# Performance work log

Hardware: AMD Instinct MI355X
Metric: run time of the kernel (lower is better)

The kernel has to match this reference:

```python
import jax, jax.numpy as jnp
import numpy as np

B = 64
SIZES = [5023, 1256, 314, 79, 20]
NV = [s + 1 for s in SIZES]          # vertex counts incl. padding vertex
K = 12                               # spiral length (all levels)
LAT = 128
ENC_F = [3, 16, 32, 64, 128]
DEC_IN = [128, 64, 32, 32, 16]
DEC_OUT = [64, 32, 32, 16, 3]


def setup_inputs() -> dict:
    keys = iter(jax.random.split(jax.random.key(0), 80))

    def nrm(shape, scale=1.0):
        return jax.random.normal(next(keys), shape, jnp.float32) * scale

    inp = {}
    inp['x_talking'] = nrm((B, NV[0], 3))
    inp['template'] = nrm((B, NV[0], 3))
    for i in range(4):
        inp['D%d' % i] = nrm((NV[i + 1], NV[i]), 1.0 / np.sqrt(NV[i]))
        inp['U%d' % i] = nrm((NV[i], NV[i + 1]), 1.0 / np.sqrt(NV[i + 1]))
    for i in range(4):
        fan = ENC_F[i] * K
        inp['enc_w%d' % i] = nrm((ENC_F[i + 1], fan), 1.0 / np.sqrt(fan))
        inp['enc_b%d' % i] = jnp.zeros((ENC_F[i + 1],), jnp.float32)
    inp['fc_enc_w'] = nrm((LAT, NV[4] * DEC_IN[0]), 1.0 / np.sqrt(NV[4] * DEC_IN[0]))
    inp['fc_enc_b'] = jnp.zeros((LAT,), jnp.float32)
    inp['fc_dec_w'] = nrm((NV[4] * DEC_IN[0], 2 * LAT), 1.0 / np.sqrt(2 * LAT))
    inp['fc_dec_b'] = jnp.zeros((NV[4] * DEC_IN[0],), jnp.float32)
    for i in range(5):
        fan = DEC_IN[i] * K
        inp['dec_w%d' % i] = nrm((DEC_OUT[i], fan), 1.0 / np.sqrt(fan))
        inp['dec_b%d' % i] = jnp.zeros((DEC_OUT[i],), jnp.float32)
    for i in range(4):
        inp['S%d' % i] = jax.random.randint(next(keys), (NV[i], K), 0, NV[i], jnp.int32)
    return inp


def _spiral_conv(x, S, W, b, act):
    # x: [B, N, F]; S: [N, K] spiral neighbor indices; W: [out, K*F] (torch Linear layout)
    Bv, Nv, F = x.shape
    g = x[:, S, :].reshape(Bv, Nv, K * F)            # spiral neighbor gather
    y = act(jnp.einsum('bnf,of->bno', g, W) + b)     # gather-GEMM + activation
    mask = jnp.ones((1, Nv, 1), y.dtype).at[0, -1, 0].set(0.0)  # zero out padding vertex
    return y * mask


def _forward(x_talking, template, D, U, enc, fc_enc_w, fc_enc_b, fc_dec_w, fc_dec_b, dec, S):
    elu = jax.nn.elu
    # encode_talking
    x = x_talking
    for i in range(4):
        x = _spiral_conv(x, S[i], enc[i][0], enc[i][1], elu)
        x = jnp.einsum('mn,bnf->bmf', D[i], x)       # downsample
    z = x.reshape(B, -1) @ fc_enc_w.T + fc_enc_b     # [B, latent]
    # decode(z, z)
    h = jnp.concatenate([z, z], axis=1) @ fc_dec_w.T + fc_dec_b
    x = h.reshape(B, NV[4], DEC_IN[0])
    for i in range(3):
        x = jnp.einsum('mn,bnf->bmf', U[3 - i], x)   # upsample
        x = _spiral_conv(x, S[3 - i], dec[i][0], dec[i][1], elu)
    x = jnp.einsum('mn,bnf->bmf', U[0], x)
    x = _spiral_conv(x, S[0], dec[3][0], dec[3][1], elu)
    x = _spiral_conv(x, S[0], dec[4][0], dec[4][1], lambda v: v)  # identity activation
    return x, x + template


def reference(x_talking, template, D0, D1, D2, D3, U0, U1, U2, U3,
              enc_w0, enc_b0, enc_w1, enc_b1, enc_w2, enc_b2, enc_w3, enc_b3,
              fc_enc_w, fc_enc_b, fc_dec_w, fc_dec_b,
              dec_w0, dec_b0, dec_w1, dec_b1, dec_w2, dec_b2, dec_w3, dec_b3, dec_w4, dec_b4,
              S0, S1, S2, S3):
    return _forward(
        x_talking, template,
        [D0, D1, D2, D3], [U0, U1, U2, U3],
        [(enc_w0, enc_b0), (enc_w1, enc_b1), (enc_w2, enc_b2), (enc_w3, enc_b3)],
        fc_enc_w, fc_enc_b, fc_dec_w, fc_dec_b,
        [(dec_w0, dec_b0), (dec_w1, dec_b1), (dec_w2, dec_b2), (dec_w3, dec_b3), (dec_w4, dec_b4)],
        [S0, S1, S2, S3])
```

## Files before the change

### kernel.cpp

```cpp
#include <hip/hip_runtime.h>
#include <cstddef>


#define BATCH 64
#define SPK 12

typedef __attribute__((ext_vector_type(8))) short bf16x8;
typedef __attribute__((ext_vector_type(4))) short bf16x4;
typedef __attribute__((ext_vector_type(4))) float f32x4;

__device__ __forceinline__ unsigned short f2bf(float x) {
    union { float f; unsigned int u; } v; v.f = x;
    unsigned int r = v.u + 0x7FFF + ((v.u >> 16) & 1);
    return (unsigned short)(r >> 16);
}

__global__ __launch_bounds__(256) void f32_to_bf16_kernel(
    const float* __restrict__ in, unsigned short* __restrict__ out, int n8)
{
    int i = blockIdx.x * 256 + threadIdx.x;
    if (i < n8) {
        const float* p = in + (size_t)i * 8;
        bf16x8 r;
#pragma unroll
        for (int j = 0; j < 8; ++j) r[j] = (short)f2bf(p[j]);
        *(bf16x8*)(out + (size_t)i * 8) = r;
    }
}

__global__ __launch_bounds__(256) void a_bf16_pad_kernel(
    const float* __restrict__ A, unsigned short* __restrict__ Ap,
    int M, int K, int Kp, int total)
{
    int i = blockIdx.x * 256 + threadIdx.x;
    if (i >= total) return;
    int kp8 = Kp >> 3;
    int m = i / kp8;
    int k0 = (i - m * kp8) * 8;
    bf16x8 r;
    if (m < M) {
        const float* src = A + (size_t)m * K + k0;
#pragma unroll
        for (int j = 0; j < 8; ++j) {
            float v = (k0 + j < K) ? src[j] : 0.f;
            r[j] = (short)f2bf(v);
        }
    } else {
#pragma unroll
        for (int j = 0; j < 8; ++j) r[j] = 0;
    }
    *(bf16x8*)(Ap + (size_t)m * Kp + k0) = r;
}

template<int LOGF, int OBF16>
__global__ __launch_bounds__(64) void conv_wmfma_kernel(
    const unsigned short* __restrict__ x, const int* __restrict__ S,
    const unsigned short* __restrict__ Wb, const float* __restrict__ bias,
    void* __restrict__ yv, int Nv, int O, int elu_flag, int swz)
{
    constexpr int F  = 1 << LOGF;
    constexpr int KF = SPK * F;
    constexpr int NS = KF / 32;
    const int lane = threadIdx.x;
    const int l15  = lane & 15;
    const int quad = lane >> 4;

    int bx = blockIdx.x, by = blockIdx.y, bz = blockIdx.z;
    if (swz) {
        const int gx = gridDim.x, gy = gridDim.y;
        const int total = gx * gy * gridDim.z;
        int bid = bx + gx * (by + gy * bz);
        const int chunk = total >> 3;
        int sid = (bid & 7) * chunk + (bid >> 3);
        bx = sid % gx; sid /= gx;
        by = sid % gy;
        bz = sid / gy;
    }

    const int n0   = bx * 16;
    const int o    = by * 16 + l15;
    const int b    = bz;
    const size_t xb = (size_t)b * Nv;

    const int n  = n0 + l15;
    const int ng = (n < Nv) ? n : 0;
    const unsigned short* wrow = Wb + (size_t)o * KF;

    f32x4 acc0 = (f32x4){0.f, 0.f, 0.f, 0.f};
    f32x4 acc1 = (f32x4){0.f, 0.f, 0.f, 0.f};
#pragma unroll
    for (int s = 0; s < NS; ++s) {
        int kf  = s * 32 + quad * 8;
        int k   = kf >> LOGF;
        int f   = kf & (F - 1);
        int src = S[ng * SPK + k];
        bf16x8 a = *(const bf16x8*)(x + ((xb + src) << LOGF) + f);
        bf16x8 w = *(const bf16x8*)(wrow + kf);
        if (s & 1) acc1 = __builtin_amdgcn_mfma_f32_16x16x32_bf16(a, w, acc1, 0, 0, 0);
        else       acc0 = __builtin_amdgcn_mfma_f32_16x16x32_bf16(a, w, acc0, 0, 0, 0);
    }
    float bv = bias[o];
#pragma unroll
    for (int reg = 0; reg < 4; ++reg) {
        int nn = n0 + quad * 4 + reg;
        if (nn >= Nv) continue;
        float v = acc0[reg] + acc1[reg] + bv;
        if (elu_flag && v <= 0.f) v = expm1f(v);
        if (nn == Nv - 1) v = 0.f;
        size_t off = ((size_t)b * Nv + nn) * O + o;
        if (OBF16) ((unsigned short*)yv)[off] = f2bf(v);
        else       ((float*)yv)[off] = v;
    }
}

template<int LOGF>
__global__ __launch_bounds__(256) void conv_mfma32_kernel(
    const unsigned short* __restrict__ x, const int* __restrict__ S,
    const unsigned short* __restrict__ Wb, const float* __restrict__ bias,
    float* __restrict__ y, int Nv, int KF, int elu_flag)
{
    constexpr int PAD = 40;
    __shared__ unsigned short Gs[2][256 * PAD];

    const int b    = blockIdx.x;
    const int n0   = blockIdx.y * 256;
    const int tid  = threadIdx.x;
    const int lane = tid & 63;
    const int wave = tid >> 6;
    const int wm   = wave * 64;
    const int l15  = lane & 15;
    const int quad = lane >> 4;
    const size_t xb = (size_t)b * Nv;
    const int nslab = KF >> 5;

    f32x4 acc[4][2];
#pragma unroll
    for (int t = 0; t < 4; ++t)
#pragma unroll
        for (int o = 0; o < 2; ++o) acc[t][o] = (f32x4){0.f, 0.f, 0.f, 0.f};

    auto gath = [&](int k0, bf16x8* g) {
        int n = n0 + tid;
        if (n < Nv) {
#pragma unroll
            for (int j = 0; j < 4; ++j) {
                int kf  = k0 + j * 8;
                int k   = kf >> LOGF;
                int f   = kf & ((1 << LOGF) - 1);
                int src = S[n * SPK + k];
                g[j] = *(const bf16x8*)(x + ((xb + src) << LOGF) + f);
            }
        } else {
#pragma unroll
            for (int j = 0; j < 4; ++j)
#pragma unroll
                for (int e = 0; e < 8; ++e) g[j][e] = 0;
        }
    };
    auto put = [&](int buf, const bf16x8* g) {
#pragma unroll
        for (int j = 0; j < 4; ++j)
            *(bf16x8*)&Gs[buf][tid * PAD + j * 8] = g[j];
    };
    auto wfrag = [&](int k0, int o16) {
        return *(const bf16x8*)(Wb + (size_t)(o16 * 16 + l15) * KF + k0 + quad * 8);
    };

    bf16x8 gcur[4], gnext[4];
    gath(0, gcur);
    put(0, gcur);
    __syncthreads();

    for (int s = 0; s < nslab; ++s) {
        const int cur = s & 1;
        const bool more = (s + 1) < nslab;
        if (more) gath((s + 1) * 32, gnext);
        bf16x8 wf0 = wfrag(s * 32, 0);
        bf16x8 wf1 = wfrag(s * 32, 1);
#pragma unroll
        for (int t = 0; t < 4; ++t) {
            bf16x8 a = *(const bf16x8*)&Gs[cur][(wm + t * 16 + l15) * PAD + quad * 8];
            acc[t][0] = __builtin_amdgcn_mfma_f32_16x16x32_bf16(a, wf0, acc[t][0], 0, 0, 0);
            acc[t][1] = __builtin_amdgcn_mfma_f32_16x16x32_bf16(a, wf1, acc[t][1], 0, 0, 0);
        }
        if (more) {
            put(cur ^ 1, gnext);
            __syncthreads();
        }
    }

    float bv0 = bias[l15];
    float bv1 = bias[16 + l15];
#pragma unroll
    for (int t = 0; t < 4; ++t)
#pragma unroll
        for (int reg = 0; reg < 4; ++reg) {
            int n = n0 + wm + t * 16 + quad * 4 + reg;
            if (n >= Nv) continue;
            float v0 = acc[t][0][reg] + bv0;
            float v1 = acc[t][1][reg] + bv1;
            if (elu_flag) {
                if (v0 <= 0.f) v0 = expm1f(v0);
                if (v1 <= 0.f) v1 = expm1f(v1);
            }
            if (n == Nv - 1) { v0 = 0.f; v1 = 0.f; }
            size_t off = ((size_t)b * Nv + n) * 32 + l15;
            y[off]      = v0;
            y[off + 16] = v1;
        }
}

__global__ __launch_bounds__(256) void dsamp_mfma3_kernel(
    const unsigned short* __restrict__ Ab, const unsigned short* __restrict__ Xt,
    float* __restrict__ Y, int M, int Kp, int logF, int kchunk,
    int atomic_flag, int swz)
{
    constexpr int PAD = 40;
    __shared__ unsigned short As[2][128 * PAD];
    __shared__ unsigned short Bs[2][128 * PAD];

    int bx = blockIdx.x, by = blockIdx.y, bz = blockIdx.z;
    if (swz) {
        const int gx = gridDim.x, gy = gridDim.y;
        const int total = gx * gy * gridDim.z;
        int bid = bx + gx * (by + gy * bz);
        const int chunk = total >> 3;
        int sid = (bid & 7) * chunk + (bid >> 3);
        bx = sid % gx; sid /= gx;
        by = sid % gy;
        bz = sid / gy;
    }

    const int fmask = (1 << logF) - 1;
    const int m0   = bx * 128;
    const int c0   = by * 128;
    const int kbeg = bz * kchunk;
    int kend = kbeg + kchunk; if (kend > Kp) kend = Kp;
    const int nslab = (kend - kbeg + 31) >> 5;

    const int tid  = threadIdx.x;
    const int lane = tid & 63;
    const int wave = tid >> 6;
    const int wm   = (wave >> 1) * 64;
    const int wn   = (wave & 1) * 64;
    const int l15  = lane & 15;
    const int quad = lane >> 4;

    const int s_row = tid >> 2;
    const int s_k8  = (tid & 3) * 8;

    f32x4 acc[4][4];
#pragma unroll
    for (int i = 0; i < 4; ++i)
#pragma unroll
        for (int j = 0; j < 4; ++j) acc[i][j] = (f32x4){0.f, 0.f, 0.f, 0.f};

    bf16x8 apre[2], bpre[2];

    auto loadAB = [&](int ko) {
        apre[0] = *(const bf16x8*)(Ab + (size_t)(m0 + s_row)      * Kp + ko + s_k8);
        apre[1] = *(const bf16x8*)(Ab + (size_t)(m0 + s_row + 64) * Kp + ko + s_k8);
        bpre[0] = *(const bf16x8*)(Xt + (size_t)(c0 + s_row)      * Kp + ko + s_k8);
        bpre[1] = *(const bf16x8*)(Xt + (size_t)(c0 + s_row + 64) * Kp + ko + s_k8);
    };
    auto stage = [&](int buf) {
        *(bf16x8*)&As[buf][s_row * PAD + s_k8]        = apre[0];
        *(bf16x8*)&As[buf][(s_row + 64) * PAD + s_k8] = apre[1];
        *(bf16x8*)&Bs[buf][s_row * PAD + s_k8]        = bpre[0];
        *(bf16x8*)&Bs[buf][(s_row + 64) * PAD + s_k8] = bpre[1];
    };

    loadAB(kbeg);
    stage(0);
    __syncthreads();

    for (int s = 0; s < nslab; ++s) {
        const int cur = s & 1;
        const bool more = (s + 1) < nslab;
        if (more) loadAB(kbeg + (s + 1) * 32);

        bf16x8 af[4], bfr[4];
#pragma unroll
        for (int t = 0; t < 4; ++t) {
            af[t]  = *(const bf16x8*)&As[cur][(wm + t * 16 + l15) * PAD + quad * 8];
            bfr[t] = *(const bf16x8*)&Bs[cur][(wn + t * 16 + l15) * PAD + quad * 8];
        }
#pragma unroll
        for (int tm = 0; tm < 4; ++tm)
#pragma unroll
            for (int tn = 0; tn < 4; ++tn)
                acc[tm][tn] = __builtin_amdgcn_mfma_f32_16x16x32_bf16(af[tm], bfr[tn], acc[tm][tn], 0, 0, 0);

        if (more) { stage(cur ^ 1); __syncthreads(); }
    }

#pragma unroll
    for (int tm = 0; tm < 4; ++tm)
#pragma unroll
        for (int tn = 0; tn < 4; ++tn)
#pragma unroll
            for (int reg = 0; reg < 4; ++reg) {
                int m  = m0 + wm + tm * 16 + quad * 4 + reg;
                int cc = c0 + wn + tn * 16 + l15;
                if (m < M) {
                    int bb = cc >> logF, f = cc & fmask;
                    float* dst = Y + (((size_t)bb * M + m) << logF) + f;
                    if (atomic_flag) atomicAdd(dst, acc[tm][tn][reg]);
                    else *dst = acc[tm][tn][reg];
                }
            }
}

__global__ __launch_bounds__(256) void dsamp_mfma2_kernel(
    const unsigned short* __restrict__ Ap, const float* __restrict__ X,
    float* __restrict__ Y, int M, int K, int Kp, int logF, int kchunk,
    int atomic_flag)
{
    constexpr int PAD = 40;
    __shared__ unsigned short Xs[2][64 * PAD];

    const int fmask = (1 << logF) - 1;
    const int m0   = blockIdx.x * 64;
    const int c0   = blockIdx.y * 64;
    const int kbeg = blockIdx.z * kchunk;
    int kend = kbeg + kchunk; if (kend > K) kend = K;
    const int nslab = (kend - kbeg + 31) >> 5;

    const int tid  = threadIdx.x;
    const int lane = tid & 63;
    const int wave = tid >> 6;
    const int wm   = (wave >> 1) * 32;
    const int wn   = (wave & 1) * 32;
    const int l15  = lane & 15;
    const int quad = lane >> 4;

    const int skk  = tid >> 4;
    const int scg  = (tid & 15) * 4;
    const int cB   = c0 + scg;
    const int xbb  = cB >> logF;
    const int xf   = cB & fmask;
    const size_t xrowbase = (((size_t)xbb * K) << logF) + xf;

    const int mA0 = m0 + wm + l15;
    const int mA1 = mA0 + 16;
    const int kaoff = quad * 8;

    f32x4 acc[2][2];
    acc[0][0] = acc[0][1] = acc[1][0] = acc[1][1] = (f32x4){0.f, 0.f, 0.f, 0.f};

    float4 xn0, xn1;
    bf16x8 ac0, ac1, an0, an1;

    {
        int k = kbeg + skk;
        xn0 = make_float4(0.f, 0.f, 0.f, 0.f);
        if (k < kend) xn0 = *(const float4*)(X + xrowbase + ((size_t)k << logF));
        k = kbeg + 16 + skk;
        xn1 = make_float4(0.f, 0.f, 0.f, 0.f);
        if (k < kend) xn1 = *(const float4*)(X + xrowbase + ((size_t)k << logF));
        int ka = kbeg + kaoff;
        ac0 = *(const bf16x8*)(Ap + (size_t)mA0 * Kp + ka);
        ac1 = *(const bf16x8*)(Ap + (size_t)mA1 * Kp + ka);
        unsigned short* p = &Xs[0][0];
        p[(scg + 0) * PAD + skk] = f2bf(xn0.x);
        p[(scg + 1) * PAD + skk] = f2bf(xn0.y);
        p[(scg + 2) * PAD + skk] = f2bf(xn0.z);
        p[(scg + 3) * PAD + skk] = f2bf(xn0.w);
        int kk1 = 16 + skk;
        p[(scg + 0) * PAD + kk1] = f2bf(xn1.x);
        p[(scg + 1) * PAD + kk1] = f2bf(xn1.y);
        p[(scg + 2) * PAD + kk1] = f2bf(xn1.z);
        p[(scg + 3) * PAD + kk1] = f2bf(xn1.w);
    }
    __syncthreads();

    for (int s = 0; s < nslab; ++s) {
        const int cur = s & 1;
        const bool more = (s + 1 < nslab);
        if (more) {
            int k0 = kbeg + (s + 1) * 32;
            int k = k0 + skk;
            xn0 = make_float4(0.f, 0.f, 0.f, 0.f);
            if (k < kend) xn0 = *(const float4*)(X + xrowbase + ((size_t)k << logF));
            k = k0 + 16 + skk;
            xn1 = make_float4(0.f, 0.f, 0.f, 0.f);
            if (k < kend) xn1 = *(const float4*)(X + xrowbase + ((size_t)k << logF));
            int ka = k0 + kaoff;
            an0 = *(const bf16x8*)(Ap + (size_t)mA0 * Kp + ka);
            an1 = *(const bf16x8*)(Ap + (size_t)mA1 * Kp + ka);
        }
        {
            const unsigned short* p = &Xs[cur][0];
            bf16x8 b0 = *(const bf16x8*)&p[(wn +      l15) * PAD + quad * 8];
            bf16x8 b1 = *(const bf16x8*)&p[(wn + 16 + l15) * PAD + quad * 8];
            acc[0][0] = __builtin_amdgcn_mfma_f32_16x16x32_bf16(ac0, b0, acc[0][0], 0, 0, 0);
            acc[0][1] = __builtin_amdgcn_mfma_f32_16x16x32_bf16(ac0, b1, acc[0][1], 0, 0, 0);
            acc[1][0] = __builtin_amdgcn_mfma_f32_16x16x32_bf16(ac1, b0, acc[1][0], 0, 0, 0);
            acc[1][1] = __builtin_amdgcn_mfma_f32_16x16x32_bf16(ac1, b1, acc[1][1], 0, 0, 0);
        }
        if (more) {
            unsigned short* q = &Xs[cur ^ 1][0];
            q[(scg + 0) * PAD + skk] = f2bf(xn0.x);
            q[(scg + 1) * PAD + skk] = f2bf(xn0.y);
            q[(scg + 2) * PAD + skk] = f2bf(xn0.z);
            q[(scg + 3) * PAD + skk] = f2bf(xn0.w);
            int kk1 = 16 + skk;
            q[(scg + 0) * PAD + kk1] = f2bf(xn1.x);
            q[(scg + 1) * PAD + kk1] = f2bf(xn1.y);
            q[(scg + 2) * PAD + kk1] = f2bf(xn1.z);
            q[(scg + 3) * PAD + kk1] = f2bf(xn1.w);
            __syncthreads();
            ac0 = an0; ac1 = an1;
        }
    }

#pragma unroll
    for (int tm = 0; tm < 2; ++tm)
#pragma unroll
        for (int tn = 0; tn < 2; ++tn)
#pragma unroll
            for (int reg = 0; reg < 4; ++reg) {
                int m  = m0 + wm + tm * 16 + quad * 4 + reg;
                int cc = c0 + wn + tn * 16 + l15;
                if (m < M) {
                    int bb = cc >> logF, f = cc & fmask;
                    float* dst = Y + (((size_t)bb * M + m) << logF) + f;
                    if (atomic_flag) atomicAdd(dst, acc[tm][tn][reg]);
                    else *dst = acc[tm][tn][reg];
                }
            }
}

template<int MT, int OT>
__global__ __launch_bounds__(256) void conv_gemm_kernel(
    const float* __restrict__ x, const int* __restrict__ S,
    const float* __restrict__ W, const float* __restrict__ bias,
    float* __restrict__ y, int Nv, int logF, int O, int KF, int KFr,
    int elu_flag)
{
    constexpr int CT = OT / 4;
    constexpr int RT = 256 / CT;
    static_assert(RT * 4 == MT, "tile shape");
    __shared__ float Gs[32][MT];
    __shared__ float Ws[32][OT];

    const int b   = blockIdx.x;
    const int n0  = blockIdx.y * MT;
    const int tid = threadIdx.x;
    const int cx  = tid % CT;
    const int ry  = tid / CT;
    const int r0  = ry * 4;
    const int o0  = cx * 4;
    const int fmask = (1 << logF) - 1;
    const size_t xb = (size_t)b * Nv;

    float acc[4][4];
#pragma unroll
    for (int i = 0; i < 4; ++i)
#pragma unroll
        for (int j = 0; j < 4; ++j) acc[i][j] = 0.f;

    for (int k0 = 0; k0 < KF; k0 += 32) {
        constexpr int GSLOTS = MT * 8;
#pragma unroll
        for (int i = 0; i < GSLOTS / 256; ++i) {
            int idx = tid + i * 256;
            int r   = idx & (MT - 1);
            int jg  = idx / MT;
            int j0  = jg * 4;
            int n   = n0 + r;
            int kf  = k0 + j0;
            float4 v = make_float4(0.f, 0.f, 0.f, 0.f);
            if (n < Nv && kf < KFr) {
                int k   = kf >> logF;
                int f   = kf & fmask;
                int src = S[n * SPK + k];
                v = *(const float4*)(x + ((xb + src) << logF) + f);
            }
            Gs[j0 + 0][r] = v.x; Gs[j0 + 1][r] = v.y;
            Gs[j0 + 2][r] = v.z; Gs[j0 + 3][r] = v.w;
        }
        constexpr int WSLOTS = OT * 8;
#pragma unroll
        for (int i = 0; i < (WSLOTS + 255) / 256; ++i) {
            int idx = tid + i * 256;
            if (WSLOTS >= 256 || idx < WSLOTS) {
                int o  = idx & (OT - 1);
                int jg = idx / OT;
                int j0 = jg * 4;
                float4 v = *(const float4*)(W + (size_t)o * KF + k0 + j0);
                Ws[j0 + 0][o] = v.x; Ws[j0 + 1][o] = v.y;
                Ws[j0 + 2][o] = v.z; Ws[j0 + 3][o] = v.w;
            }
        }
        __syncthreads();
#pragma unroll
        for (int kk = 0; kk < 32; ++kk) {
            float4 g = *(const float4*)&Gs[kk][r0];
            float4 w = *(const float4*)&Ws[kk][o0];
            acc[0][0] += g.x * w.x; acc[0][1] += g.x * w.y; acc[0][2] += g.x * w.z; acc[0][3] += g.x * w.w;
            acc[1][0] += g.y * w.x; acc[1][1] += g.y * w.y; acc[1][2] += g.y * w.z; acc[1][3] += g.y * w.w;
            acc[2][0] += g.z * w.x; acc[2][1] += g.z * w.y; acc[2][2] += g.z * w.z; acc[2][3] += g.z * w.w;
            acc[3][0] += g.w * w.x; acc[3][1] += g.w * w.y; acc[3][2] += g.w * w.z; acc[3][3] += g.w * w.w;
        }
        __syncthreads();
    }

    float4 bv = *(const float4*)(bias + o0);
#pragma unroll
    for (int i = 0; i < 4; ++i) {
        int n = n0 + r0 + i;
        if (n >= Nv) continue;
        float v0 = acc[i][0] + bv.x;
        float v1 = acc[i][1] + bv.y;
        float v2 = acc[i][2] + bv.z;
        float v3 = acc[i][3] + bv.w;
        if (elu_flag) {
            v0 = v0 > 0.f ? v0 : expm1f(v0);
            v1 = v1 > 0.f ? v1 : expm1f(v1);
            v2 = v2 > 0.f ? v2 : expm1f(v2);
            v3 = v3 > 0.f ? v3 : expm1f(v3);
        }
        if (n == Nv - 1) { v0 = v1 = v2 = v3 = 0.f; }
        *(float4*)(y + ((size_t)b * Nv + n) * O + o0) = make_float4(v0, v1, v2, v3);
    }
}

template<int OBF16>
__global__ __launch_bounds__(256) void dsamp_kernel(
    const float* __restrict__ A, const float* __restrict__ X,
    void* __restrict__ Yv, int M, int N, int F)
{
    __shared__ float As[16][68];
    __shared__ float Xs[16][64];

    const int m0  = blockIdx.x * 64;
    const int c0  = blockIdx.y * 64;
    const int tid = threadIdx.x;
    const int tx  = tid & 15;
    const int ty  = tid >> 4;

    float acc[4][4];
#pragma unroll
    for (int i = 0; i < 4; ++i)
#pragma unroll
        for (int j = 0; j < 4; ++j) acc[i][j] = 0.f;

    for (int k0 = 0; k0 < N; k0 += 16) {
#pragma unroll
        for (int p = 0; p < 4; ++p) {
            int r  = (tid >> 4) + p * 16;
            int kk = tid & 15;
            int m  = m0 + r;
            int n  = k0 + kk;
            float v = 0.f;
            if (m < M && n < N) v = A[(size_t)m * N + n];
            As[kk][r] = v;
        }
        {
            int kk = tid >> 4;
            int cc = (tid & 15) * 4;
            int n  = k0 + kk;
            float4 v = make_float4(0.f, 0.f, 0.f, 0.f);
            if (n < N) {
                int c  = c0 + cc;
                int bb = c / F;
                int f  = c - bb * F;
                v = *(const float4*)(X + ((size_t)bb * N + n) * F + f);
            }
            *(float4*)&Xs[kk][cc] = v;
        }
        __syncthreads();
#pragma unroll
        for (int kk = 0; kk < 16; ++kk) {
            float4 av = *(const float4*)&As[kk][ty * 4];
            float4 xv = *(const float4*)&Xs[kk][tx * 4];
            acc[0][0] += av.x * xv.x; acc[0][1] += av.x * xv.y; acc[0][2] += av.x * xv.z; acc[0][3] += av.x * xv.w;
            acc[1][0] += av.y * xv.x; acc[1][1] += av.y * xv.y; acc[1][2] += av.y * xv.z; acc[1][3] += av.y * xv.w;
            acc[2][0] += av.z * xv.x; acc[2][1] += av.z * xv.y; acc[2][2] += av.z * xv.z; acc[2][3] += av.z * xv.w;
            acc[3][0] += av.w * xv.x; acc[3][1] += av.w * xv.y; acc[3][2] += av.w * xv.z; acc[3][3] += av.w * xv.w;
        }
        __syncthreads();
    }

    const int cbase = c0 + tx * 4;
    const int bb = cbase / F;
    const int f  = cbase - bb * F;
#pragma unroll
    for (int i = 0; i < 4; ++i) {
        int m = m0 + ty * 4 + i;
        if (m < M) {
            size_t off = ((size_t)bb * M + m) * F + f;
            if (OBF16) {
                bf16x4 v;
                v[0] = (short)f2bf(acc[i][0]); v[1] = (short)f2bf(acc[i][1]);
                v[2] = (short)f2bf(acc[i][2]); v[3] = (short)f2bf(acc[i][3]);
                *(bf16x4*)((unsigned short*)Yv + off) = v;
            } else {
                *(float4*)((float*)Yv + off) =
                    make_float4(acc[i][0], acc[i][1], acc[i][2], acc[i][3]);
            }
        }
    }
}

__global__ __launch_bounds__(256) void fc_wave_kernel(
    const float* __restrict__ in, const float* __restrict__ W,
    const float* __restrict__ bias, float* __restrict__ out,
    int In, int O, int dup)
{
    const int gw   = blockIdx.x * 4 + (threadIdx.x >> 6);
    const int lane = threadIdx.x & 63;
    const int b = gw / O;
    const int o = gw - b * O;
    const float* xr = in + (size_t)b * In;
    float acc = 0.f;
    if (dup) {
        const float* wr = W + (size_t)o * (2 * In);
        for (int k = lane; k < In; k += 64)
            acc += xr[k] * (wr[k] + wr[In + k]);
    } else {
        const float* wr = W + (size_t)o * In;
        for (int k = lane; k < In; k += 64)
            acc += xr[k] * wr[k];
    }
#pragma unroll
    for (int off = 32; off > 0; off >>= 1)
        acc += __shfl_down(acc, off, 64);
    if (lane == 0) out[(size_t)b * O + o] = acc + bias[o];
}

__global__ __launch_bounds__(256) void xpose_bf16_kernel(
    const float* __restrict__ x, unsigned short* __restrict__ xt,
    int K, int Kp, int logF)
{
    const int c  = blockIdx.y * 256 + threadIdx.x;
    const int k0 = blockIdx.x * 8;
    const int bb = c >> logF;
    const int f  = c & ((1 << logF) - 1);
    const float* src = x + (((size_t)bb * K) << logF) + f;
    bf16x8 r;
#pragma unroll
    for (int j = 0; j < 8; ++j) {
        int k = k0 + j;
        float v = (k < K) ? src[(size_t)k << logF] : 0.f;
        r[j] = (short)f2bf(v);
    }
    *(bf16x8*)(xt + (size_t)c * Kp + k0) = r;
}

__global__ __launch_bounds__(256) void pad_e0_w_kernel(
    const float* __restrict__ w, float* __restrict__ wp)
{
    int i = blockIdx.x * 256 + threadIdx.x;
    if (i < 1024) {
        int o = i >> 6, kf = i & 63;
        int k = kf >> 2, f = kf & 3;
        wp[i] = (f < 3 && k < 12) ? w[o * 36 + k * 3 + f] : 0.f;
    }
}
__global__ __launch_bounds__(256) void pad_x4_kernel(
    const float* __restrict__ x, float* __restrict__ xp, int n)
{
    int i = blockIdx.x * 256 + threadIdx.x;
    if (i < n) {
        int f = i & 3, nb = i >> 2;
        xp[i] = (f < 3) ? x[nb * 3 + f] : 0.f;
    }
}
__global__ __launch_bounds__(256) void pad_c4_w_kernel(
    const float* __restrict__ w, const float* __restrict__ b,
    float* __restrict__ wp, float* __restrict__ bp)
{
    int i = blockIdx.x * 256 + threadIdx.x;
    if (i < 3072) {
        int o = i / 192;
        wp[i] = (o < 3) ? w[i] : 0.f;
    }
    if (i < 16) bp[i] = (i < 3) ? b[i] : 0.f;
}
__global__ __launch_bounds__(256) void extract_add_kernel(
    const float* __restrict__ cp, const float* __restrict__ t,
    float* __restrict__ o0, float* __restrict__ o1, int n)
{
    int i = blockIdx.x * 256 + threadIdx.x;
    if (i < n) {
        int f = i % 3, nb = i / 3;
        float v = cp[(size_t)nb * 16 + f];
        o0[i] = v;
        o1[i] = v + t[i];
    }
}


static inline int ilog2(int v) { int l = 0; while ((1 << l) < v) ++l; return l; }

static inline void a_bf16_launch(const float* A, unsigned short* Ap, int M, int K,
                                 int Mp, int Kp, hipStream_t s)
{
    int total = Mp * (Kp >> 3);
    a_bf16_pad_kernel<<<(total + 255) / 256, 256, 0, s>>>(A, Ap, M, K, Kp, total);
}

static inline void dsamp_mfma2_launch(const unsigned short* Ap, const float* X,
                                      float* Y, int M, int K, int Kp, int F,
                                      int ks, hipStream_t s)
{
    int kchunk = (K + ks - 1) / ks;
    kchunk = (kchunk + 31) & ~31;
    int ksz = (K + kchunk - 1) / kchunk;
    dim3 grid((M + 63) / 64, F, ksz);
    dsamp_mfma2_kernel<<<grid, 256, 0, s>>>(Ap, X, Y, M, K, Kp, ilog2(F), kchunk,
                                            ksz > 1 ? 1 : 0);
}

static inline void dsamp_mfma3_launch(const unsigned short* Ab, const unsigned short* Xt,
                                      float* Y, int M, int Kp, int F,
                                      int ks, hipStream_t s)
{
    int slabs = Kp >> 5;
    int kchunk = ((slabs + ks - 1) / ks) * 32;
    int ksz = (Kp + kchunk - 1) / kchunk;
    int gx = (M + 127) / 128, gy = (BATCH * F) / 128;
    int total = gx * gy * ksz;
    int swz = (ksz > 1 && (total & 7) == 0) ? 1 : 0;
    dim3 grid(gx, gy, ksz);
    dsamp_mfma3_kernel<<<grid, 256, 0, s>>>(Ab, Xt, Y, M, Kp, ilog2(F), kchunk,
                                            ksz > 1 ? 1 : 0, swz);
}

template<int OBF16>
static inline void dsamp_launch(const float* A, const float* X, void* Y,
                                int M, int N, int F, hipStream_t s)
{
    dim3 grid((M + 63) / 64, F);
    dsamp_kernel<OBF16><<<grid, 256, 0, s>>>(A, X, Y, M, N, F);
}

extern "C" void kernel_launch(void* const* d_in, const int* in_sizes, int n_in,
                              void* d_out, int out_size, void* d_ws, size_t ws_size,
                              hipStream_t stream)
{
    const float* x_talking = (const float*)d_in[0];
    const float* templ     = (const float*)d_in[1];
    const float* D0 = (const float*)d_in[2];
    const float* U0 = (const float*)d_in[3];
    const float* D1 = (const float*)d_in[4];
    const float* U1 = (const float*)d_in[5];
    const float* D2 = (const float*)d_in[6];
    const float* U2 = (const float*)d_in[7];
    const float* D3 = (const float*)d_in[8];
    const float* U3 = (const float*)d_in[9];
    const float* enc_w0 = (const float*)d_in[10]; const float* enc_b0 = (const float*)d_in[11];
    const float* enc_w1 = (const float*)d_in[12]; const float* enc_b1 = (const float*)d_in[13];
    const float* enc_w2 = (const float*)d_in[14]; const float* enc_b2 = (const float*)d_in[15];
    const float* enc_w3 = (const float*)d_in[16]; const float* enc_b3 = (const float*)d_in[17];
    const float* fc_enc_w = (const float*)d_in[18]; const float* fc_enc_b = (const float*)d_in[19];
    const float* fc_dec_w = (const float*)d_in[20]; const float* fc_dec_b = (const float*)d_in[21];
    const float* dec_w0 = (const float*)d_in[22]; const float* dec_b0 = (const float*)d_in[23];
    const float* dec_w1 = (const float*)d_in[24]; const float* dec_b1 = (const float*)d_in[25];
    const float* dec_w2 = (const float*)d_in[26]; const float* dec_b2 = (const float*)d_in[27];
    const float* dec_w3 = (const float*)d_in[28]; const float* dec_b3 = (const float*)d_in[29];
    const float* dec_w4 = (const float*)d_in[30]; const float* dec_b4 = (const float*)d_in[31];
    const int* S0 = (const int*)d_in[32];
    const int* S1 = (const int*)d_in[33];
    const int* S2 = (const int*)d_in[34];
    const int* S3 = (const int*)d_in[35];

    float* bufA = (float*)d_ws;
    float* bufB = bufA + 10289152;

    float* out0 = (float*)d_out;
    float* out1 = out0 + 964608;

    unsigned short* Xt_e0 = (unsigned short*)(bufB + 1290240);
    unsigned short* Xt_c2 = (unsigned short*)bufB;
    unsigned short* U0b   = (unsigned short*)(bufB + 1400000);
    unsigned short* Wb_e2 = (unsigned short*)(bufB + 4700000);
    unsigned short* Wb_e3 = (unsigned short*)(bufB + 4715000);
    unsigned short* Wb_c0 = (unsigned short*)(bufB + 4765000);
    unsigned short* Wb_c1 = (unsigned short*)(bufB + 4815000);
    float* xpad   = bufA + 5200000;
    float* WpE0   = bufA + 6600000;
    unsigned short* D0b   = (unsigned short*)(bufA + 6700000);
    unsigned short* D1b   = (unsigned short*)(bufA + 9950000);
    unsigned short* U1b   = (unsigned short*)(bufA + 4000000);
    unsigned short* Wb_e1 = (unsigned short*)(bufA + 10160000);
    unsigned short* Wb_c2 = (unsigned short*)(bufA + 10170000);
    unsigned short* Xb_e1   = (unsigned short*)(bufA + 5200000);
    unsigned short* Xb_e2   = (unsigned short*)(bufA + 2000000);
    unsigned short* Xb_c2in = (unsigned short*)(bufA + 2600000);
    unsigned short* Xb_c3 = (unsigned short*)bufB;
    unsigned short* Xb_c4 = (unsigned short*)(bufA + 5200000);
    unsigned short* Wb_c3 = (unsigned short*)bufA;
    float* WpC4   = bufA + 10000;
    float* BpC4   = bufA + 13500;
    unsigned short* Wb_c4 = (unsigned short*)(bufA + 14000);

    hipMemsetAsync(bufB, 0, (size_t)1287168 * sizeof(float), stream);

    pad_e0_w_kernel<<<4, 256, 0, stream>>>(enc_w0, WpE0);
    pad_x4_kernel<<<5024, 256, 0, stream>>>(x_talking, xpad, 1286144);
    a_bf16_launch(D0, D0b, 1257, 5024, 1280, 5024, stream);
    a_bf16_launch(D1, D1b, 315, 1257, 320, 1280, stream);
    f32_to_bf16_kernel<<<3, 256, 0, stream>>>(enc_w1, Wb_e1, 768);
    f32_to_bf16_kernel<<<6, 256, 0, stream>>>(dec_w2, Wb_c2, 1536);
    f32_to_bf16_kernel<<<12, 256, 0, stream>>>(enc_w2, Wb_e2, 3072);
    f32_to_bf16_kernel<<<48, 256, 0, stream>>>(enc_w3, Wb_e3, 12288);
    f32_to_bf16_kernel<<<48, 256, 0, stream>>>(dec_w0, Wb_c0, 12288);
    f32_to_bf16_kernel<<<12, 256, 0, stream>>>(dec_w1, Wb_c1, 3072);

    {
        dim3 grid(BATCH, (5024 + 255) / 256);
        conv_gemm_kernel<256, 16><<<grid, 256, 0, stream>>>(
            xpad, S0, WpE0, enc_b0, bufA, 5024, 2, 16, 64, 48, 1);
    }
    xpose_bf16_kernel<<<dim3(628, 4), 256, 0, stream>>>(bufA, Xt_e0, 5024, 5024, 4);
    dsamp_mfma3_launch(D0b, Xt_e0, bufB, 1257, 5024, 16, 8, stream);
    f32_to_bf16_kernel<<<629, 256, 0, stream>>>(bufB, Xb_e1, 160896);
    a_bf16_launch(U0, U0b, 5024, 1257, 5120, 1280, stream);
    a_bf16_launch(U1, U1b, 1257, 315, 1280, 320, stream);
    {
        dim3 grid(BATCH, (1257 + 255) / 256);
        conv_mfma32_kernel<4><<<grid, 256, 0, stream>>>(
            Xb_e1, S1, Wb_e1, enc_b1, bufA, 1257, 192, 1);
    }
    hipMemsetAsync(bufB, 0, (size_t)645120 * sizeof(float), stream);
    dsamp_mfma2_launch(D1b, bufA, bufB, 315, 1257, 1280, 32, 8, stream);
    f32_to_bf16_kernel<<<315, 256, 0, stream>>>(bufB, Xb_e2, 80640);
    {
        dim3 grid((315 + 15) / 16, 64 / 16, BATCH);
        conv_wmfma_kernel<5, 0><<<grid, 64, 0, stream>>>(
            Xb_e2, S2, Wb_e2, enc_b2, bufA, 315, 64, 1, 0);
    }
    dsamp_launch<1>(D2, bufA, bufB, 80, 315, 64, stream);
    {
        dim3 grid((80 + 15) / 16, 128 / 16, BATCH);
        conv_wmfma_kernel<6, 0><<<grid, 64, 0, stream>>>(
            (const unsigned short*)bufB, S3, Wb_e3, enc_b3, bufA, 80, 128, 1, 0);
    }
    dsamp_launch<0>(D3, bufA, bufB, 21, 80, 128, stream);

    fc_wave_kernel<<<dim3((BATCH * 128) / 4), 256, 0, stream>>>(bufB, fc_enc_w, fc_enc_b, bufA, 2688, 128, 0);
    fc_wave_kernel<<<dim3((BATCH * 2688) / 4), 256, 0, stream>>>(bufA, fc_dec_w, fc_dec_b, bufB, 128, 2688, 1);

    dsamp_launch<1>(U3, bufB, bufA, 80, 21, 128, stream);
    {
        dim3 grid((80 + 15) / 16, 64 / 16, BATCH);
        conv_wmfma_kernel<7, 0><<<grid, 64, 0, stream>>>(
            (const unsigned short*)bufA, S3, Wb_c0, dec_b0, bufB, 80, 64, 1, 0);
    }
    dsamp_launch<1>(U2, bufB, bufA, 315, 80, 64, stream);
    {
        dim3 grid((315 + 15) / 16, 32 / 16, BATCH);
        conv_wmfma_kernel<6, 0><<<grid, 64, 0, stream>>>(
            (const unsigned short*)bufA, S2, Wb_c1, dec_b1, bufB, 315, 32, 1, 0);
    }
    dsamp_mfma2_launch(U1b, bufB, bufA, 1257, 315, 320, 32, 1, stream);
    f32_to_bf16_kernel<<<1257, 256, 0, stream>>>(bufA, Xb_c2in, 321792);
    {
        dim3 grid(BATCH, (1257 + 255) / 256);
        conv_mfma32_kernel<5><<<grid, 256, 0, stream>>>(
            Xb_c2in, S1, Wb_c2, dec_b2, bufA, 1257, 384, 1);
    }
    xpose_bf16_kernel<<<dim3(160, 8), 256, 0, stream>>>(bufA, Xt_c2, 1257, 1280, 5);
    dsamp_mfma3_launch(U0b, Xt_c2, bufA, 5024, 1280, 32, 1, stream);

    f32_to_bf16_kernel<<<5024, 256, 0, stream>>>(bufA, Xb_c3, 1286144);
    f32_to_bf16_kernel<<<3, 256, 0, stream>>>(dec_w3, Wb_c3, 768);
    pad_c4_w_kernel<<<12, 256, 0, stream>>>(dec_w4, dec_b4, WpC4, BpC4);
    f32_to_bf16_kernel<<<2, 256, 0, stream>>>(WpC4, Wb_c4, 384);
    {
        dim3 grid((5024 + 15) / 16, 1, BATCH);
        conv_wmfma_kernel<5, 1><<<grid, 64, 0, stream>>>(
            Xb_c3, S0, Wb_c3, dec_b3, (void*)Xb_c4, 5024, 16, 1, 1);
    }
    {
        dim3 grid((5024 + 15) / 16, 1, BATCH);
        conv_wmfma_kernel<4, 0><<<grid, 64, 0, stream>>>(
            Xb_c4, S0, Wb_c4, BpC4, (void*)bufB, 5024, 16, 0, 1);
    }
    extract_add_kernel<<<(964608 + 255) / 256, 256, 0, stream>>>(bufB, templ, out0, out1, 964608);
}
```

Baseline: 747.4 us.

## Stage spiral gathers in LDS and prefragment weights for final decoder convs

Adds a new conv kernel for the last two full-resolution decoder spiral convs. It gathers the 12 neighbor rows for 16 vertices into padded shared memory using shuffled spiral indices, then feeds MFMA from LDS with two alternating accumulators. A small kernel pre-permutes the weights into per-lane MFMA fragment order so each lane loads them contiguously. This targets gather latency and uncoalesced weight loads, at the cost of two extra tiny launches and a dependence on 5024 being divisible by 16.

Measured after the change: 717.0 us. 4.1% less time.

```diff
diff --git a/kernel.cpp b/kernel.cpp
--- a/kernel.cpp
+++ b/kernel.cpp
@@ -50,6 +50,113 @@
         for (int j = 0; j < 8; ++j) r[j] = 0;
     }
     *(bf16x8*)(Ap + (size_t)m * Kp + k0) = r;
+}
+
+__global__ __launch_bounds__(256) void w_frag16_kernel(
+    const unsigned short* __restrict__ Wb, unsigned short* __restrict__ Wfs,
+    int KF, int total)
+{
+    int i = blockIdx.x * 256 + threadIdx.x;
+    if (i >= total) return;
+    int j    = i & 7;
+    int lane = (i >> 3) & 63;
+    int s    = i >> 9;
+    int l15  = lane & 15;
+    int quad = (lane >> 4) & 3;
+    Wfs[i] = Wb[l15 * KF + s * 32 + quad * 8 + j];
+}
+
+template<int LOGF, int OBF16>
+__global__ __launch_bounds__(64, 4) void conv_cmfma_kernel(
+    const unsigned short* __restrict__ x, const int* __restrict__ S,
+    const unsigned short* __restrict__ Wfs, const float* __restrict__ bias,
+    void* __restrict__ yv, int Nv, int elu_flag, int swz)
+{
+    constexpr int F     = 1 << LOGF;
+    constexpr int KF    = SPK * F;
+    constexpr int NS    = KF / 32;
+    constexpr int RPADu = (LOGF == 5) ? 40 : 24;
+    __shared__ unsigned short Gs[12 * 16 * RPADu];
+
+    const int lane = threadIdx.x;
+    const int l15  = lane & 15;
+    const int quad = (lane >> 4) & 3;
+
+    int bx = blockIdx.x, bz = blockIdx.z;
+    if (swz) {
+        const int gx = gridDim.x;
+        const int total = gx * gridDim.z;
+        int bid = bx + gx * bz;
+        const int chunk = total >> 3;
+        int sid = (bid & 7) * chunk + (bid >> 3);
+        bx = sid % gx;
+        bz = sid / gx;
+    }
+    const int n0 = bx * 16;
+    const int b  = bz;
+    const size_t xb = (size_t)b * Nv;
+
+    int4 sv;
+    {
+        int g = lane >> 4; if (g > 2) g = 2;
+        int n = n0 + l15; if (n >= Nv) n = 0;
+        sv = *(const int4*)(S + n * SPK + g * 4);
+    }
+
+    if constexpr (LOGF == 5) {
+        const int grow = lane >> 2, gchk = lane & 3;
+#pragma unroll
+        for (int k = 0; k < 12; ++k) {
+            int sel = ((k >> 2) << 4) | grow;
+            int comp = k & 3;
+            int src = (comp == 0) ? __shfl(sv.x, sel)
+                    : (comp == 1) ? __shfl(sv.y, sel)
+                    : (comp == 2) ? __shfl(sv.z, sel)
+                                  : __shfl(sv.w, sel);
+            bf16x8 v = *(const bf16x8*)(x + ((xb + src) << 5) + gchk * 8);
+            *(bf16x8*)&Gs[k * 16 * RPADu + grow * RPADu + gchk * 8] = v;
+        }
+    } else {
+        const int khalf = lane >> 5, grow = (lane >> 1) & 15, gchk = lane & 1;
+#pragma unroll
+        for (int g = 0; g < 6; ++g) {
+            int k0 = 2 * g;
+            int sel0 = ((k0 >> 2) << 4) | grow;
+            int sel1 = (((k0 + 1) >> 2) << 4) | grow;
+            int s0 = ((k0 & 3) == 0) ? __shfl(sv.x, sel0) : __shfl(sv.z, sel0);
+            int s1 = (((k0 + 1) & 3) == 1) ? __shfl(sv.y, sel1) : __shfl(sv.w, sel1);
+            int src = khalf ? s1 : s0;
+            int k   = k0 + khalf;
+            bf16x8 v = *(const bf16x8*)(x + ((xb + src) << 4) + gchk * 8);
+            *(bf16x8*)&Gs[k * 16 * RPADu + grow * RPADu + gchk * 8] = v;
+        }
+    }
+
+    f32x4 acc0 = (f32x4){0.f, 0.f, 0.f, 0.f};
+    f32x4 acc1 = (f32x4){0.f, 0.f, 0.f, 0.f};
+#pragma unroll
+    for (int s = 0; s < NS; ++s) {
+        int kf = s * 32 + quad * 8;
+        int k  = kf >> LOGF;
+        int f  = kf & (F - 1);
+        bf16x8 a = *(const bf16x8*)&Gs[k * 16 * RPADu + l15 * RPADu + f];
+        bf16x8 w = *(const bf16x8*)(Wfs + (s * 64 + lane) * 8);
+        if (s & 1) acc1 = __builtin_amdgcn_mfma_f32_16x16x32_bf16(a, w, acc1, 0, 0, 0);
+        else       acc0 = __builtin_amdgcn_mfma_f32_16x16x32_bf16(a, w, acc0, 0, 0, 0);
+    }
+
+    float bv = bias[l15];
+#pragma unroll
+    for (int reg = 0; reg < 4; ++reg) {
+        int nn = n0 + quad * 4 + reg;
+        if (nn >= Nv) continue;
+        float v = acc0[reg] + acc1[reg] + bv;
+        if (elu_flag && v <= 0.f) v = expm1f(v);
+        if (nn == Nv - 1) v = 0.f;
+        size_t off = ((size_t)b * Nv + nn) * 16 + l15;
+        if (OBF16) ((unsigned short*)yv)[off] = f2bf(v);
+        else       ((float*)yv)[off] = v;
+    }
 }
 
 template<int LOGF, int OBF16>
@@ -795,7 +902,9 @@
     unsigned short* Wb_c3 = (unsigned short*)bufA;
     float* WpC4   = bufA + 10000;
     float* BpC4   = bufA + 13500;
-    unsigned short* Wb_c4 = (unsigned short*)(bufA + 14000);
+    unsigned short* Wb_c4  = (unsigned short*)(bufA + 14000);
+    unsigned short* Wfs_c3 = (unsigned short*)(bufA + 16000);
+    unsigned short* Wfs_c4 = (unsigned short*)(bufA + 20000);
 
     hipMemsetAsync(bufB, 0, (size_t)1287168 * sizeof(float), stream);
 
@@ -868,17 +977,19 @@
 
     f32_to_bf16_kernel<<<5024, 256, 0, stream>>>(bufA, Xb_c3, 1286144);
     f32_to_bf16_kernel<<<3, 256, 0, stream>>>(dec_w3, Wb_c3, 768);
+    w_frag16_kernel<<<24, 256, 0, stream>>>(Wb_c3, Wfs_c3, 384, 6144);
     pad_c4_w_kernel<<<12, 256, 0, stream>>>(dec_w4, dec_b4, WpC4, BpC4);
     f32_to_bf16_kernel<<<2, 256, 0, stream>>>(WpC4, Wb_c4, 384);
-    {
-        dim3 grid((5024 + 15) / 16, 1, BATCH);
-        conv_wmfma_kernel<5, 1><<<grid, 64, 0, stream>>>(
-            Xb_c3, S0, Wb_c3, dec_b3, (void*)Xb_c4, 5024, 16, 1, 1);
-    }
-    {
-        dim3 grid((5024 + 15) / 16, 1, BATCH);
-        conv_wmfma_kernel<4, 0><<<grid, 64, 0, stream>>>(
-            Xb_c4, S0, Wb_c4, BpC4, (void*)bufB, 5024, 16, 0, 1);
+    w_frag16_kernel<<<12, 256, 0, stream>>>(Wb_c4, Wfs_c4, 192, 3072);
+    {
+        dim3 grid(5024 / 16, 1, BATCH);
+        conv_cmfma_kernel<5, 1><<<grid, 64, 0, stream>>>(
+            Xb_c3, S0, Wfs_c3, dec_b3, (void*)Xb_c4, 5024, 1, 1);
+    }
+    {
+        dim3 grid(5024 / 16, 1, BATCH);
+        conv_cmfma_kernel<4, 0><<<grid, 64, 0, stream>>>(
+            Xb_c4, S0, Wfs_c4, BpC4, (void*)bufB, 5024, 0, 1);
     }
     extract_add_kernel<<<(964608 + 255) / 256, 256, 0, stream>>>(bufB, templ, out0, out1, 964608);
 }
```
